# Performance work log

Measured on AMD Instinct MI355X. Metric: run time of the kernel, lower is better.

Reference implementation:

```python
import jax, jax.numpy as jnp
import numpy as np

N_HIDDEN = 1024
N_INPUTS = 8
N_OUTPUTS = 8
BATCH = 32
SEQ_LEN = 1000
DT = 0.001
TAU = 0.01
TAU_DEPR = 0.2
TAU_FACIL = 1.5
BETA = 10.0
PROB_C = 0.1


def setup_inputs() -> dict:
    key = jax.random.key(0)
    ks = jax.random.split(key, 9)
    # gain adjustment from source: 1/(0.5/(1+beta*0.5*tau_depr)) = 4.0 -> gain = 6.4
    gain = 1.6 * (1.0 / (0.5 / (1.0 + BETA * 0.5 * TAU_DEPR)))
    x = jax.random.normal(ks[0], (BATCH, SEQ_LEN, N_INPUTS), dtype=jnp.float32)
    h_0 = jax.random.normal(ks[1], (BATCH, N_HIDDEN), dtype=jnp.float32)
    r_0 = jax.random.uniform(ks[2], (BATCH, N_HIDDEN), dtype=jnp.float32)
    u_0 = jax.random.uniform(ks[3], (BATCH, N_HIDDEN), dtype=jnp.float32)
    p_rel = jax.random.uniform(ks[4], (N_HIDDEN,), minval=0.1, maxval=0.9, dtype=jnp.float32)
    presyn_scaling = jnp.ones((N_HIDDEN,), dtype=jnp.float32)
    W_ih = jax.random.normal(ks[5], (N_HIDDEN, N_INPUTS), dtype=jnp.float32) / np.sqrt(N_HIDDEN)
    W_hh = jax.random.normal(ks[6], (N_HIDDEN, N_HIDDEN), dtype=jnp.float32) * (gain / np.sqrt(PROB_C * N_HIDDEN))
    W_hh_mask = jax.random.bernoulli(ks[7], PROB_C, (N_HIDDEN, N_HIDDEN)).astype(jnp.float32)
    W_hz = jax.random.normal(ks[8], (N_OUTPUTS, N_HIDDEN), dtype=jnp.float32) / np.sqrt(N_HIDDEN)
    return {"x": x, "h_0": h_0, "r_0": r_0, "u_0": u_0, "p_rel": p_rel,
            "presyn_scaling": presyn_scaling, "W_ih": W_ih, "W_hh": W_hh,
            "W_hh_mask": W_hh_mask, "W_hz": W_hz}


def reference(x, h_0, r_0, u_0, p_rel, presyn_scaling, W_ih, W_hh, W_hh_mask, W_hz):
    # noise_std = 0.0 in source -> noise term is identically zero.
    W_eff = W_hh * W_hh_mask                       # [n, n], eff[i,j] applied to presyn j
    x_proj = jnp.einsum('bti,ni->btn', x, W_ih)    # precompute input drive [b, t, n]

    def step(carry, x_t):
        h_prev, r_prev, u_prev, h_tr = carry       # each [b, n]
        drive = 0.5 * (1.0 + h_tr)                 # presynaptic activity
        r_t = r_prev + ((p_rel - r_prev) / TAU_DEPR - BETA * r_prev * drive) * DT
        u_t = u_prev + ((p_rel - u_prev) / TAU_FACIL + BETA * (1.0 - u_prev) * drive) * DT
        # h_tr @ (r_prev * scal * W_hh * mask).T == (r_prev * scal * h_tr) @ W_eff.T
        rec = (r_prev * presyn_scaling * h_tr) @ W_eff.T
        h_t = h_prev + ((-h_prev + x_t + rec) / TAU) * DT
        h_tr_new = jnp.tanh(h_t)
        z_t = h_tr_new @ W_hz.T                    # [b, n_outputs]
        return (h_t, r_t, u_t, h_tr_new), (z_t, h_t, r_t, u_t)

    init = (h_0, r_0, u_0, jnp.tanh(h_0))
    _, (z, h, r, u) = jax.lax.scan(step, init, jnp.swapaxes(x_proj, 0, 1))
    # scan stacks on time axis 0 -> transpose back to [b, t, ...]
    to_bt = lambda a: jnp.swapaxes(a, 0, 1)
    return (to_bt(z), to_bt(h), to_bt(r), to_bt(u))
```

## Files before the change

### kernel.cpp

```cpp
#include <hip/hip_runtime.h>
#include <math.h>

#define NH 1024
#define NB 32
#define NI 8
#define NO 8
#define TSTEPS 1000

#define NWG 256
#define BLK 512
#define NG 8
#define NM 32
#define GBATCH 4

#define OFF_Z 0
#define OFF_H (NB * TSTEPS * NO)
#define OFF_R (OFF_H + NB * TSTEPS * NH)
#define OFF_U (OFF_R + NB * TSTEPS * NH)

#define WS_A  8192
#define WS_ZP (WS_A + 2 * NG * NH * GBATCH)

typedef unsigned long long u64;

__device__ __forceinline__ float2 aload2(const float* p) {
    u64 v = __hip_atomic_load((const u64*)p, __ATOMIC_RELAXED,
                              __HIP_MEMORY_SCOPE_AGENT);
    return __builtin_bit_cast(float2, v);
}
__device__ __forceinline__ float aload1(const float* p) {
    return __hip_atomic_load(p, __ATOMIC_RELAXED, __HIP_MEMORY_SCOPE_AGENT);
}
__device__ __forceinline__ void astore(float* p, float v) {
    __hip_atomic_store(p, v, __ATOMIC_RELAXED, __HIP_MEMORY_SCOPE_AGENT);
}

__global__ __launch_bounds__(BLK, 2) void rnn_stp_kernel(
    const float* __restrict__ x,
    const float* __restrict__ h0,
    const float* __restrict__ r0,
    const float* __restrict__ u0,
    const float* __restrict__ prel,
    const float* __restrict__ scal,
    const float* __restrict__ Wih,
    const float* __restrict__ Whh,
    const float* __restrict__ Wmask,
    const float* __restrict__ Whz,
    float* __restrict__ out,
    float* __restrict__ ws)
{
    const int tid = threadIdx.x;
    const int g   = blockIdx.x;

    const int G = g & 7;
    const int m = g >> 3;

    unsigned* slot = (unsigned*)ws;
    float* Abuf = ws + WS_A;
    float* ZP   = ws + WS_ZP;

    const int ib = 32 * m;

    __shared__ float4 atile[NM * 33];
    __shared__ float  red[8 * 16 * 9];
    __shared__ float  wzlds[NM * 8];

    const int lane = tid & 63, wid = tid >> 6;

    if (tid < NM * 8)
        wzlds[(tid >> 3) * 8 + (tid & 7)] = Whz[(tid & 7) * NH + ib + (tid >> 3)];

    const int ks = tid >> 4;
    const int il = tid & 15;

    float w[2][32];
    #pragma unroll
    for (int nn = 0; nn < 2; ++nn) {
        const int row = 32 * m + il + 16 * nn;
        const float* wp = Whh   + row * NH + 32 * ks;
        const float* mp = Wmask + row * NH + 32 * ks;
        #pragma unroll
        for (int jj = 0; jj < 32; ++jj) w[nn][jj] = wp[jj] * mp[jj];
    }

    const bool own = tid < 128;
    const int ob = tid >> 5;
    const int on = tid & 31;
    const int bglob = G * GBATCH + ob;
    const int oi = ib + on;
    float h = 0.f, r = 0.f, u = 0.f, htr = 0.f, p = 0.f, sc = 0.f;
    float wih[8];
    if (own) {
        h  = h0[bglob * NH + oi];
        r  = r0[bglob * NH + oi];
        u  = u0[bglob * NH + oi];
        p  = prel[oi];
        sc = scal[oi];
        #pragma unroll
        for (int k = 0; k < 8; ++k) wih[k] = Wih[oi * NI + k];
        htr = tanhf(h);
        astore(&Abuf[G * (NH * GBATCH) + oi * GBATCH + ob], r * sc * htr);
    }

    const int bf = m >> 3, of = m & 7;

    __syncthreads();
    if (tid == 0)
        __hip_atomic_store(&slot[(G * NM + m) * 32], 1u,
                           __ATOMIC_RELAXED, __HIP_MEMORY_SCOPE_AGENT);

    const unsigned* myslot = &slot[(G * NM + 4 * wid + (lane & 3)) * 32];

    for (int t = 0; t < TSTEPS; ++t) {
        const int par = t & 1;

        if (lane < 4) {
            while (__hip_atomic_load(myslot, __ATOMIC_RELAXED,
                                     __HIP_MEMORY_SCOPE_AGENT) < (unsigned)(t + 1))
                __builtin_amdgcn_s_sleep(1);
        }

        const float* Ag = Abuf + par * (NG * NH * GBATCH) + G * (NH * GBATCH);
        {
            float2 s0 = aload2(Ag + tid * 8 + 0);
            float2 s1 = aload2(Ag + tid * 8 + 2);
            float2 s2 = aload2(Ag + tid * 8 + 4);
            float2 s3 = aload2(Ag + tid * 8 + 6);
            const int r0i = tid * 2;
            atile[r0i + (r0i >> 5)]     = make_float4(s0.x, s0.y, s1.x, s1.y);
            atile[r0i + 1 + (r0i >> 5)] = make_float4(s2.x, s2.y, s3.x, s3.y);
        }

        float4 xa = make_float4(0.f, 0.f, 0.f, 0.f), xb = xa;
        if (own) {
            const float4* xp = (const float4*)(x + (bglob * TSTEPS + t) * NI);
            xa = xp[0];
            xb = xp[1];
        }
        __syncthreads();

        float zfin = 0.f;
        if (t >= 1 && wid == 4 && lane < NM)
            zfin = aload1(ZP + (par ^ 1) * (NG * GBATCH * NO * NM)
                          + G * (GBATCH * NO * NM)
                          + bf * (NO * NM) + of * NM + lane);

        float acc[2][4] = {{0.f,0.f,0.f,0.f},{0.f,0.f,0.f,0.f}};
        {
            const float4* at4 = atile + 33 * ks;
            #pragma unroll
            for (int jj = 0; jj < 32; ++jj) {
                float4 a = at4[jj];
                const float w0 = w[0][jj], w1 = w[1][jj];
                acc[0][0] = fmaf(a.x, w0, acc[0][0]);
                acc[0][1] = fmaf(a.y, w0, acc[0][1]);
                acc[0][2] = fmaf(a.z, w0, acc[0][2]);
                acc[0][3] = fmaf(a.w, w0, acc[0][3]);
                acc[1][0] = fmaf(a.x, w1, acc[1][0]);
                acc[1][1] = fmaf(a.y, w1, acc[1][1]);
                acc[1][2] = fmaf(a.z, w1, acc[1][2]);
                acc[1][3] = fmaf(a.w, w1, acc[1][3]);
            }
        }

        #pragma unroll
        for (int mm = 16; mm <= 32; mm <<= 1) {
            #pragma unroll
            for (int nn = 0; nn < 2; ++nn) {
                #pragma unroll
                for (int q = 0; q < 4; ++q)
                    acc[nn][q] += __shfl_xor(acc[nn][q], mm, 64);
            }
        }
        if (lane < 16) {
            float* rp = red + (wid * 16 + lane) * 9;
            rp[0] = acc[0][0]; rp[1] = acc[0][1];
            rp[2] = acc[0][2]; rp[3] = acc[0][3];
            rp[4] = acc[1][0]; rp[5] = acc[1][1];
            rp[6] = acc[1][2]; rp[7] = acc[1][3];
        }

        if (t >= 1 && wid == 4) {
            zfin += __shfl_xor(zfin, 1, 64);
            zfin += __shfl_xor(zfin, 2, 64);
            zfin += __shfl_xor(zfin, 4, 64);
            zfin += __shfl_xor(zfin, 8, 64);
            zfin += __shfl_xor(zfin, 16, 64);
            if (lane == 0)
                out[OFF_Z + ((G * GBATCH + bf) * TSTEPS + (t - 1)) * NO + of] = zfin;
        }
        __syncthreads();

        if (own) {
            float rec = 0.f;
            #pragma unroll
            for (int wv = 0; wv < 8; ++wv)
                rec += red[(wv * 16 + (on & 15)) * 9 + (on >> 4) * 4 + ob];

            float xv = fmaf(xa.x, wih[0], fmaf(xa.y, wih[1],
                       fmaf(xa.z, wih[2], xa.w * wih[3])));
            xv = fmaf(xb.x, wih[4], fmaf(xb.y, wih[5],
                 fmaf(xb.z, wih[6], fmaf(xb.w, wih[7], xv))));

            float drive = 0.5f * (1.0f + htr);
            float rn = r + ((p - r) / 0.2f - 10.0f * r * drive) * 0.001f;
            float un = u + ((p - u) / 1.5f + 10.0f * (1.0f - u) * drive) * 0.001f;
            float hn = h + ((-h + xv + rec) / 0.01f) * 0.001f;
            float htn = tanhf(hn);

            out[OFF_H + (bglob * TSTEPS + t) * NH + oi] = hn;
            out[OFF_R + (bglob * TSTEPS + t) * NH + oi] = rn;
            out[OFF_U + (bglob * TSTEPS + t) * NH + oi] = un;

            astore(&Abuf[(par ^ 1) * (NG * NH * GBATCH) + G * (NH * GBATCH)
                         + oi * GBATCH + ob], rn * sc * htn);

            float zp[8];
            #pragma unroll
            for (int o = 0; o < 8; ++o) zp[o] = htn * wzlds[on * 8 + o];
            #pragma unroll
            for (int mm = 1; mm <= 16; mm <<= 1) {
                #pragma unroll
                for (int o = 0; o < 8; ++o)
                    zp[o] += __shfl_xor(zp[o], mm, 64);
            }
            if (on == 0) {
                float* zpp = ZP + par * (NG * GBATCH * NO * NM)
                             + G * (GBATCH * NO * NM) + ob * (NO * NM) + m;
                #pragma unroll
                for (int o = 0; o < 8; ++o) astore(zpp + o * NM, zp[o]);
            }

            h = hn; r = rn; u = un; htr = htn;
        }

        __syncthreads();
        if (tid == 0)
            __hip_atomic_store(&slot[(G * NM + m) * 32], (unsigned)(t + 2),
                               __ATOMIC_RELAXED, __HIP_MEMORY_SCOPE_AGENT);
    }

    if (lane < 4) {
        while (__hip_atomic_load(myslot, __ATOMIC_RELAXED,
                                 __HIP_MEMORY_SCOPE_AGENT) < (unsigned)(TSTEPS + 1))
            __builtin_amdgcn_s_sleep(1);
    }
    __syncthreads();
    if (wid == 4) {
        float v = 0.f;
        if (lane < NM)
            v = aload1(ZP + 1 * (NG * GBATCH * NO * NM)
                       + G * (GBATCH * NO * NM)
                       + bf * (NO * NM) + of * NM + lane);
        v += __shfl_xor(v, 1, 64);
        v += __shfl_xor(v, 2, 64);
        v += __shfl_xor(v, 4, 64);
        v += __shfl_xor(v, 8, 64);
        v += __shfl_xor(v, 16, 64);
        if (lane == 0)
            out[OFF_Z + ((G * GBATCH + bf) * TSTEPS + 999) * NO + of] = v;
    }
}

extern "C" void kernel_launch(void* const* d_in, const int* in_sizes, int n_in,
                              void* d_out, int out_size, void* d_ws, size_t ws_size,
                              hipStream_t stream) {
    const float* x     = (const float*)d_in[0];
    const float* h0    = (const float*)d_in[1];
    const float* r0    = (const float*)d_in[2];
    const float* u0    = (const float*)d_in[3];
    const float* prel  = (const float*)d_in[4];
    const float* scal  = (const float*)d_in[5];
    const float* Wih   = (const float*)d_in[6];
    const float* Whh   = (const float*)d_in[7];
    const float* Wmask = (const float*)d_in[8];
    const float* Whz   = (const float*)d_in[9];
    float* out = (float*)d_out;
    float* ws  = (float*)d_ws;

    hipMemsetAsync(d_ws, 0, NWG * 128, stream);

    void* args[] = { &x, &h0, &r0, &u0, &prel, &scal,
                     &Wih, &Whh, &Wmask, &Whz, &out, &ws };
    hipLaunchCooperativeKernel((void*)rnn_stp_kernel, dim3(NWG), dim3(BLK),
                               args, 0, stream);
}
```

Before: 4.216 ms.

## Replace flag-slot barrier with sequence-tagged 64-bit packed data exchange

Each exchanged float is now packed with a step counter into one 64-bit atomic word, so consumers poll the data itself until every tag reaches the required step. This removes the per-workgroup flag slots, the end-of-step __syncthreads and the flag store, so each wavefront waits only on the values it actually reads. The global h/r/u output stores move after the exchange stores so they do not delay publishing. The cost is twice the exchange bytes, a larger workspace memset, and the risk of spinning on many cache lines instead of a single flag.

```diff
diff --git a/kernel.cpp b/kernel.cpp
--- a/kernel.cpp
+++ b/kernel.cpp
@@ -18,21 +18,23 @@
 #define OFF_R (OFF_H + NB * TSTEPS * NH)
 #define OFF_U (OFF_R + NB * TSTEPS * NH)
 
-#define WS_A  8192
-#define WS_ZP (WS_A + 2 * NG * NH * GBATCH)
+#define APK_SZ (2 * NG * NH * GBATCH)
+#define ZPK_SZ (2 * NG * GBATCH * NO * NM)
 
 typedef unsigned long long u64;
-
-__device__ __forceinline__ float2 aload2(const float* p) {
-    u64 v = __hip_atomic_load((const u64*)p, __ATOMIC_RELAXED,
-                              __HIP_MEMORY_SCOPE_AGENT);
-    return __builtin_bit_cast(float2, v);
-}
-__device__ __forceinline__ float aload1(const float* p) {
+typedef unsigned int u32;
+
+__device__ __forceinline__ u64 aload64(const u64* p) {
     return __hip_atomic_load(p, __ATOMIC_RELAXED, __HIP_MEMORY_SCOPE_AGENT);
 }
-__device__ __forceinline__ void astore(float* p, float v) {
+__device__ __forceinline__ void astore64(u64* p, u64 v) {
     __hip_atomic_store(p, v, __ATOMIC_RELAXED, __HIP_MEMORY_SCOPE_AGENT);
+}
+__device__ __forceinline__ u64 packvs(float f, u32 s) {
+    return (u64)__builtin_bit_cast(u32, f) | ((u64)s << 32);
+}
+__device__ __forceinline__ float unpackf(u64 v) {
+    return __builtin_bit_cast(float, (u32)v);
 }
 
 __global__ __launch_bounds__(BLK, 2) void rnn_stp_kernel(
@@ -55,9 +57,8 @@
     const int G = g & 7;
     const int m = g >> 3;
 
-    unsigned* slot = (unsigned*)ws;
-    float* Abuf = ws + WS_A;
-    float* ZP   = ws + WS_ZP;
+    u64* Apk = (u64*)ws;
+    u64* ZPk = Apk + APK_SZ;
 
     const int ib = 32 * m;
 
@@ -99,37 +100,14 @@
         #pragma unroll
         for (int k = 0; k < 8; ++k) wih[k] = Wih[oi * NI + k];
         htr = tanhf(h);
-        astore(&Abuf[G * (NH * GBATCH) + oi * GBATCH + ob], r * sc * htr);
+        astore64(&Apk[G * (NH * GBATCH) + oi * GBATCH + ob],
+                 packvs(r * sc * htr, 1u));
     }
 
     const int bf = m >> 3, of = m & 7;
-
-    __syncthreads();
-    if (tid == 0)
-        __hip_atomic_store(&slot[(G * NM + m) * 32], 1u,
-                           __ATOMIC_RELAXED, __HIP_MEMORY_SCOPE_AGENT);
-
-    const unsigned* myslot = &slot[(G * NM + 4 * wid + (lane & 3)) * 32];
 
     for (int t = 0; t < TSTEPS; ++t) {
         const int par = t & 1;
-
-        if (lane < 4) {
-            while (__hip_atomic_load(myslot, __ATOMIC_RELAXED,
-                                     __HIP_MEMORY_SCOPE_AGENT) < (unsigned)(t + 1))
-                __builtin_amdgcn_s_sleep(1);
-        }
-
-        const float* Ag = Abuf + par * (NG * NH * GBATCH) + G * (NH * GBATCH);
-        {
-            float2 s0 = aload2(Ag + tid * 8 + 0);
-            float2 s1 = aload2(Ag + tid * 8 + 2);
-            float2 s2 = aload2(Ag + tid * 8 + 4);
-            float2 s3 = aload2(Ag + tid * 8 + 6);
-            const int r0i = tid * 2;
-            atile[r0i + (r0i >> 5)]     = make_float4(s0.x, s0.y, s1.x, s1.y);
-            atile[r0i + 1 + (r0i >> 5)] = make_float4(s2.x, s2.y, s3.x, s3.y);
-        }
 
         float4 xa = make_float4(0.f, 0.f, 0.f, 0.f), xb = xa;
         if (own) {
@@ -137,13 +115,35 @@
             xa = xp[0];
             xb = xp[1];
         }
+
+        const u64* Ap = Apk + par * (NG * NH * GBATCH) + G * (NH * GBATCH)
+                        + tid * 8;
+        const u32 need = (u32)(t + 1);
+        u64 v0, v1, v2, v3, v4, v5, v6, v7;
+        for (;;) {
+            v0 = aload64(Ap + 0); v1 = aload64(Ap + 1);
+            v2 = aload64(Ap + 2); v3 = aload64(Ap + 3);
+            v4 = aload64(Ap + 4); v5 = aload64(Ap + 5);
+            v6 = aload64(Ap + 6); v7 = aload64(Ap + 7);
+            u32 s = (u32)(v0 >> 32);
+            u32 s1 = (u32)(v1 >> 32); s = s1 < s ? s1 : s;
+            u32 s2 = (u32)(v2 >> 32); s = s2 < s ? s2 : s;
+            u32 s3 = (u32)(v3 >> 32); s = s3 < s ? s3 : s;
+            u32 s4 = (u32)(v4 >> 32); s = s4 < s ? s4 : s;
+            u32 s5 = (u32)(v5 >> 32); s = s5 < s ? s5 : s;
+            u32 s6 = (u32)(v6 >> 32); s = s6 < s ? s6 : s;
+            u32 s7 = (u32)(v7 >> 32); s = s7 < s ? s7 : s;
+            if (s >= need) break;
+            __builtin_amdgcn_s_sleep(1);
+        }
+        {
+            const int r0i = tid * 2;
+            atile[r0i + (r0i >> 5)] =
+                make_float4(unpackf(v0), unpackf(v1), unpackf(v2), unpackf(v3));
+            atile[r0i + 1 + (r0i >> 5)] =
+                make_float4(unpackf(v4), unpackf(v5), unpackf(v6), unpackf(v7));
+        }
         __syncthreads();
-
-        float zfin = 0.f;
-        if (t >= 1 && wid == 4 && lane < NM)
-            zfin = aload1(ZP + (par ^ 1) * (NG * GBATCH * NO * NM)
-                          + G * (GBATCH * NO * NM)
-                          + bf * (NO * NM) + of * NM + lane);
 
         float acc[2][4] = {{0.f,0.f,0.f,0.f},{0.f,0.f,0.f,0.f}};
         {
@@ -179,17 +179,30 @@
             rp[4] = acc[1][0]; rp[5] = acc[1][1];
             rp[6] = acc[1][2]; rp[7] = acc[1][3];
         }
+        __syncthreads();
 
         if (t >= 1 && wid == 4) {
-            zfin += __shfl_xor(zfin, 1, 64);
-            zfin += __shfl_xor(zfin, 2, 64);
-            zfin += __shfl_xor(zfin, 4, 64);
-            zfin += __shfl_xor(zfin, 8, 64);
-            zfin += __shfl_xor(zfin, 16, 64);
+            float zv = 0.f;
+            if (lane < NM) {
+                const u64* zp = ZPk + (par ^ 1) * (NG * GBATCH * NO * NM)
+                                + G * (GBATCH * NO * NM)
+                                + bf * (NO * NM) + of * NM + lane;
+                u64 vz;
+                for (;;) {
+                    vz = aload64(zp);
+                    if ((u32)(vz >> 32) >= (u32)t) break;
+                    __builtin_amdgcn_s_sleep(1);
+                }
+                zv = unpackf(vz);
+            }
+            zv += __shfl_xor(zv, 1, 64);
+            zv += __shfl_xor(zv, 2, 64);
+            zv += __shfl_xor(zv, 4, 64);
+            zv += __shfl_xor(zv, 8, 64);
+            zv += __shfl_xor(zv, 16, 64);
             if (lane == 0)
-                out[OFF_Z + ((G * GBATCH + bf) * TSTEPS + (t - 1)) * NO + of] = zfin;
-        }
-        __syncthreads();
+                out[OFF_Z + ((G * GBATCH + bf) * TSTEPS + (t - 1)) * NO + of] = zv;
+        }
 
         if (own) {
             float rec = 0.f;
@@ -208,12 +221,9 @@
             float hn = h + ((-h + xv + rec) / 0.01f) * 0.001f;
             float htn = tanhf(hn);
 
-            out[OFF_H + (bglob * TSTEPS + t) * NH + oi] = hn;
-            out[OFF_R + (bglob * TSTEPS + t) * NH + oi] = rn;
-            out[OFF_U + (bglob * TSTEPS + t) * NH + oi] = un;
-
-            astore(&Abuf[(par ^ 1) * (NG * NH * GBATCH) + G * (NH * GBATCH)
-                         + oi * GBATCH + ob], rn * sc * htn);
+            astore64(&Apk[(par ^ 1) * (NG * NH * GBATCH) + G * (NH * GBATCH)
+                          + oi * GBATCH + ob],
+                     packvs(rn * sc * htn, (u32)(t + 2)));
 
             float zp[8];
             #pragma unroll
@@ -225,40 +235,42 @@
                     zp[o] += __shfl_xor(zp[o], mm, 64);
             }
             if (on == 0) {
-                float* zpp = ZP + par * (NG * GBATCH * NO * NM)
-                             + G * (GBATCH * NO * NM) + ob * (NO * NM) + m;
+                u64* zpp = ZPk + par * (NG * GBATCH * NO * NM)
+                           + G * (GBATCH * NO * NM) + ob * (NO * NM) + m;
                 #pragma unroll
-                for (int o = 0; o < 8; ++o) astore(zpp + o * NM, zp[o]);
-            }
+                for (int o = 0; o < 8; ++o)
+                    astore64(zpp + o * NM, packvs(zp[o], (u32)(t + 1)));
+            }
+
+            out[OFF_H + (bglob * TSTEPS + t) * NH + oi] = hn;
+            out[OFF_R + (bglob * TSTEPS + t) * NH + oi] = rn;
+            out[OFF_U + (bglob * TSTEPS + t) * NH + oi] = un;
 
             h = hn; r = rn; u = un; htr = htn;
         }
-
-        __syncthreads();
-        if (tid == 0)
-            __hip_atomic_store(&slot[(G * NM + m) * 32], (unsigned)(t + 2),
-                               __ATOMIC_RELAXED, __HIP_MEMORY_SCOPE_AGENT);
-    }
-
-    if (lane < 4) {
-        while (__hip_atomic_load(myslot, __ATOMIC_RELAXED,
-                                 __HIP_MEMORY_SCOPE_AGENT) < (unsigned)(TSTEPS + 1))
-            __builtin_amdgcn_s_sleep(1);
-    }
-    __syncthreads();
+    }
+
     if (wid == 4) {
-        float v = 0.f;
-        if (lane < NM)
-            v = aload1(ZP + 1 * (NG * GBATCH * NO * NM)
-                       + G * (GBATCH * NO * NM)
-                       + bf * (NO * NM) + of * NM + lane);
-        v += __shfl_xor(v, 1, 64);
-        v += __shfl_xor(v, 2, 64);
-        v += __shfl_xor(v, 4, 64);
-        v += __shfl_xor(v, 8, 64);
-        v += __shfl_xor(v, 16, 64);
+        float zv = 0.f;
+        if (lane < NM) {
+            const u64* zp = ZPk + 1 * (NG * GBATCH * NO * NM)
+                            + G * (GBATCH * NO * NM)
+                            + bf * (NO * NM) + of * NM + lane;
+            u64 vz;
+            for (;;) {
+                vz = aload64(zp);
+                if ((u32)(vz >> 32) >= (u32)TSTEPS) break;
+                __builtin_amdgcn_s_sleep(1);
+            }
+            zv = unpackf(vz);
+        }
+        zv += __shfl_xor(zv, 1, 64);
+        zv += __shfl_xor(zv, 2, 64);
+        zv += __shfl_xor(zv, 4, 64);
+        zv += __shfl_xor(zv, 8, 64);
+        zv += __shfl_xor(zv, 16, 64);
         if (lane == 0)
-            out[OFF_Z + ((G * GBATCH + bf) * TSTEPS + 999) * NO + of] = v;
+            out[OFF_Z + ((G * GBATCH + bf) * TSTEPS + 999) * NO + of] = zv;
     }
 }
 
@@ -278,7 +290,7 @@
     float* out = (float*)d_out;
     float* ws  = (float*)d_ws;
 
-    hipMemsetAsync(d_ws, 0, NWG * 128, stream);
+    hipMemsetAsync(d_ws, 0, (size_t)(APK_SZ + ZPK_SZ) * sizeof(u64), stream);
 
     void* args[] = { &x, &h0, &r0, &u0, &prel, &scal,
                      &Wih, &Whh, &Wmask, &Whz, &out, &ws };
```

After: 9.085 ms. 2.15x slower.
